# Optimization experiments

Measured on AMD Instinct MI355X. Metric: run time of the kernel, lower is better.

The kernel has to match this reference:

```python
import jax, jax.numpy as jnp
import numpy as np
import math

INPUT_FRAMES = 12
FUTURE_FRAMES = 26
T_STEPS = INPUT_FRAMES + FUTURE_FRAMES - 1  # 37
HD = 64   # hidden_dim
D = 16    # d_attn
CIN = 3   # input channels (time='stable')
COUT = 2  # output_dim
H, W = 24, 48


def conv2d(x, w, b, pad):
    # x: (N,C,H,W), w: (O,I,kh,kw)
    y = jax.lax.conv_general_dilated(x, w, (1, 1), [(pad, pad), (pad, pad)],
                                     dimension_numbers=('NCHW', 'OIHW', 'NCHW'))
    return y + b[None, :, None, None]


def spatial_attn(q, k, v):
    # q,k,v: (N,C,S); attention over spatial dim S
    scale = 1.0 / math.sqrt(q.shape[1])
    scores = jnp.einsum('ncs,nct->nst', q, k) * scale  # (N,S,S)
    a = jax.nn.softmax(scores, axis=-1)
    return jnp.einsum('nst,nct->ncs', a, v)


def setup_inputs() -> dict:
    key = jax.random.key(0)
    ks = jax.random.split(key, 8)
    s = 0.05
    inp = {
        'input_x': jax.random.normal(ks[0], (16, T_STEPS, H, W, CIN), dtype=jnp.float32),
        # ConvLSTM gate conv: in = CIN+HD, out = 4*HD, 3x3
        'conv_w': jax.random.normal(ks[1], (4 * HD, CIN + HD, 3, 3), dtype=jnp.float32) * s,
        'conv_b': jnp.zeros((4 * HD,), jnp.float32),
        # SA memory module
        'h_w': jax.random.normal(ks[2], (3 * D, HD, 1, 1), dtype=jnp.float32) * s,
        'h_b': jnp.zeros((3 * D,), jnp.float32),
        'm_w': jax.random.normal(ks[3], (2 * D, HD, 1, 1), dtype=jnp.float32) * s,
        'm_b': jnp.zeros((2 * D,), jnp.float32),
        'z_w': jax.random.normal(ks[4], (D, 2 * D, 1, 1), dtype=jnp.float32) * s,
        'z_b': jnp.zeros((D,), jnp.float32),
        'o_w': jax.random.normal(ks[5], (3 * HD, HD + D, 3, 3), dtype=jnp.float32) * s,
        'o_b': jnp.zeros((3 * HD,), jnp.float32),
        # final 1x1 projection to output_dim
        'out_w': jax.random.normal(ks[6], (COUT, HD, 1, 1), dtype=jnp.float32) * s,
        'out_b': jnp.zeros((COUT,), jnp.float32),
    }
    return inp


def reference(input_x, conv_w, conv_b, h_w, h_b, m_w, m_b, z_w, z_b, o_w, o_b, out_w, out_b):
    x = jnp.transpose(input_x, (0, 1, 4, 2, 3))  # (N,T,C,H,W)
    N = x.shape[0]
    S = H * W

    h0 = jnp.zeros((N, HD, H, W), x.dtype)
    carry0 = (h0, h0, h0, jnp.zeros((N, COUT, H, W), x.dtype))

    def step(carry, inp_t):
        h, c, m, prev_out = carry
        xt, t = inp_t  # xt: (N,CIN,H,W), t: scalar
        autoreg = jnp.concatenate([prev_out, xt[:, 2:]], axis=1)
        feed = jnp.where(t < INPUT_FRAMES, xt, autoreg)
        # ConvLSTM gates
        comb = conv2d(jnp.concatenate([feed, h], axis=1), conv_w, conv_b, 1)
        ci, cf, co, cg = jnp.split(comb, 4, axis=1)
        i = jax.nn.sigmoid(ci)
        f = jax.nn.sigmoid(cf)
        o = jax.nn.sigmoid(co)
        g = jnp.tanh(cg)
        c = f * c + i * g
        h = o * jnp.tanh(c)
        # self-attention memory
        hq, hk, hv = jnp.split(conv2d(h, h_w, h_b, 0), 3, axis=1)
        mk, mv = jnp.split(conv2d(m, m_w, m_b, 0), 2, axis=1)
        Zh = spatial_attn(hq.reshape(N, D, S), hk.reshape(N, D, S), hv.reshape(N, D, S))
        Zm = spatial_attn(hq.reshape(N, D, S), mk.reshape(N, D, S), mv.reshape(N, D, S))
        Z = conv2d(jnp.concatenate([Zh.reshape(N, D, H, W), Zm.reshape(N, D, H, W)], axis=1), z_w, z_b, 0)
        iog = conv2d(jnp.concatenate([Z, h], axis=1), o_w, o_b, 1)
        si, sg, so = jnp.split(iog, 3, axis=1)
        si = jax.nn.sigmoid(si)
        sg = jnp.tanh(sg)
        m = si * sg + (1.0 - si) * m
        h = jax.nn.sigmoid(so) * m
        out = conv2d(h, out_w, out_b, 0)
        return (h, c, m, out), out

    xs = (jnp.transpose(x, (1, 0, 2, 3, 4)), jnp.arange(T_STEPS))
    _, outs = jax.lax.scan(step, carry0, xs)
    outputs = jnp.transpose(outs, (1, 0, 2, 3, 4))  # (N,T,COUT,H,W)

    nino = outputs[:, -FUTURE_FRAMES:, 0, 10:13, 19:30].mean(axis=(2, 3))  # (N,26)
    nino_pred = (nino[:, :-2] + nino[:, 1:-1] + nino[:, 2:]) / 3.0          # (N,24)
    return outputs, nino_pred
```

## Files before the change

### kernel.cpp

```cpp
#include <hip/hip_runtime.h>
#include <math.h>

#define HD 64
#define DATT 16
#define NCIN 3
#define NCOUT 2
#define HH 24
#define WW 48
#define SS (HH*WW)
#define NB 16
#define TSTEPS 37
#define INPUT_FRAMES 12

#define PR 26
#define PC 52
#define PHW (PR*PC)

#define OFF_H     0
#define OFF_C     1384448
#define OFF_M     2564096
#define OFF_FEED  3743744
#define OFF_Z     3808640
#define ZERO_END  4154752
#define OFF_QKV   4154752
#define OFF_MKV   5039488
#define OFF_HB    5629312
#define OFF_IOG   8873344
#define OFF_BF2   12412288
#define OFF_BF    12596864

typedef __attribute__((ext_vector_type(8))) short short8;
typedef __attribute__((ext_vector_type(4))) float f32x4;

__device__ __forceinline__ float sigmoidf_(float x) {
    return 1.0f / (1.0f + __expf(-x));
}
__device__ __forceinline__ unsigned short f2bf(float f) {
    unsigned u = __float_as_uint(f);
    unsigned r = (u + 0x7fffu + ((u >> 16) & 1u)) >> 16;
    return (unsigned short)r;
}
__device__ __forceinline__ float bf2f(unsigned short b) {
    return __uint_as_float(((unsigned)b) << 16);
}
__device__ __forceinline__ unsigned packbf(float f) {
    unsigned short hi = f2bf(f);
    unsigned short lo = f2bf(f - bf2f(hi));
    return ((unsigned)lo << 16) | (unsigned)hi;
}
__device__ __forceinline__ float unpackbf(unsigned pk) {
    return __uint_as_float(pk << 16) + __uint_as_float(pk & 0xffff0000u);
}
__device__ __forceinline__ unsigned cvt_pk_bf16(float a, float b) {
    unsigned r;
    asm("v_cvt_pk_bf16_f32 %0, %1, %2" : "=v"(r) : "v"(a), "v"(b));
    return r;
}
__device__ __forceinline__ int permrow(int t) {
    int kb = t >> 5, tl = t & 31;
    int quad = tl >> 3, rr = tl & 7;
    return kb * 32 + ((rr >= 4) ? 16 : 0) + quad * 4 + (rr & 3);
}

#define MKFRAG(P0, P1, ah, al) do {                                  \
    ah.i[0] = (P0.y << 16) | (P0.x & 0xffff);                        \
    ah.i[1] = (P0.w << 16) | (P0.z & 0xffff);                        \
    ah.i[2] = (P1.y << 16) | (P1.x & 0xffff);                        \
    ah.i[3] = (P1.w << 16) | (P1.z & 0xffff);                        \
    al.i[0] = (P0.y & 0xffff0000) | ((unsigned)P0.x >> 16);          \
    al.i[1] = (P0.w & 0xffff0000) | ((unsigned)P0.z >> 16);          \
    al.i[2] = (P1.y & 0xffff0000) | ((unsigned)P1.x >> 16);          \
    al.i[3] = (P1.w & 0xffff0000) | ((unsigned)P1.z >> 16);          \
} while (0)

__global__ void k_zero(float* __restrict__ p, int n4) {
    int i = blockIdx.x * blockDim.x + threadIdx.x;
    if (i < n4) ((float4*)p)[i] = make_float4(0.f, 0.f, 0.f, 0.f);
}

__global__ void k_prep_bf2(const float* __restrict__ cw, unsigned short* __restrict__ bbuf) {
    int idx = blockIdx.x * 256 + threadIdx.x;
    if (idx >= 344064) return;
    int j    = idx & 7;
    int lane = (idx >> 3) & 63;
    int ki   = (idx >> 9) % 21;
    int nt   = (idx / 10752) % 16;
    int p    = idx / 172032;
    int k = ki * 32 + (lane >> 4) * 8 + j;
    int ncol = nt * 16 + (lane & 15);
    unsigned short v = 0;
    if (k < 648) {
        int c = k % 72, kt = k / 72;
        if (c < 67) {
            float w = cw[ncol * 603 + c * 9 + kt];
            unsigned short hi = f2bf(w);
            v = (p == 0) ? hi : f2bf(w - bf2f(hi));
        }
    }
    bbuf[idx] = v;
}

__global__ void k_prep_bf(const float* __restrict__ ow, unsigned short* __restrict__ bbuf) {
    int idx = blockIdx.x * 256 + threadIdx.x;
    if (idx >= 282624) return;
    int j    = idx & 7;
    int lane = (idx >> 3) & 63;
    int ki   = (idx >> 9) % 23;
    int nt   = (idx / 11776) % 12;
    int p    = idx / 141312;
    int k = ki * 32 + (lane >> 4) * 8 + j;
    int ncol = nt * 16 + (lane & 15);
    unsigned short v = 0;
    if (k < 720) {
        int c = k % 80, kt = k / 80;
        float w = ow[ncol * 720 + c * 9 + kt];
        unsigned short hi = f2bf(w);
        v = (p == 0) ? hi : f2bf(w - bf2f(hi));
    }
    bbuf[idx] = v;
}

__global__ void k_feed0(const float* __restrict__ x, unsigned* __restrict__ feed) {
    int i = blockIdx.x * blockDim.x + threadIdx.x;
    if (i >= NB * 3 * SS) return;
    int s = i % SS;
    int ch = (i / SS) % 3;
    int n = i / (3 * SS);
    int y = s / WW, xx = s % WW;
    float v = x[(((size_t)(n * TSTEPS + 0) * HH + y) * WW + xx) * NCIN + ch];
    feed[((size_t)(n * 3 + ch) * PR + (y + 1)) * PC + (xx + 1)] = packbf(v);
}

#define ASTR2 76
#define ZOFF2 (3*52*ASTR2)
__global__ __launch_bounds__(256) void k_conv_lstm_mfma(
    const unsigned* __restrict__ feed, const unsigned* __restrict__ hin,
    const unsigned short* __restrict__ bbuf, const float* __restrict__ cb,
    float* __restrict__ c, unsigned* __restrict__ hout)
{
    __shared__ __align__(16) int lds[3 * 52 * ASTR2 + 8];
    const int y0 = blockIdx.x;
    const int nb = blockIdx.y;
    const int n  = blockIdx.z;
    const int tid = threadIdx.x;

    const unsigned* fbase = feed + (size_t)n * 3 * PHW;
    const unsigned* hbase = hin + (size_t)n * HD * PHW;
    for (int e = tid; e < 2808; e += 256) {
        int grp = e / 156;
        int r2  = e - grp * 156;
        int pr = r2 / 52, pc = r2 - pr * 52;
        int cc0 = grp * 4;
        int vv[4];
#pragma unroll
        for (int j = 0; j < 4; ++j) {
            int cc = cc0 + j;
            int t = 0;
            if (cc < 3)        t = (int)fbase[(size_t)cc * PHW + (y0 + pr) * PC + pc];
            else if (cc < 67)  t = (int)hbase[(size_t)(cc - 3) * PHW + (y0 + pr) * PC + pc];
            vv[j] = t;
        }
        int4 v; v.x = vv[0]; v.y = vv[1]; v.z = vv[2]; v.w = vv[3];
        *(int4*)&lds[r2 * ASTR2 + cc0] = v;
    }
    if (tid < 8) lds[ZOFF2 + tid] = 0;
    __syncthreads();

    const int wv = tid >> 6;
    const int lane = tid & 63;
    const int mcol = lane & 15;
    const int quad = lane >> 4;

    f32x4 acc[2][3];
#pragma unroll
    for (int jg = 0; jg < 2; ++jg)
#pragma unroll
        for (int xt = 0; xt < 3; ++xt) acc[jg][xt] = (f32x4){0.f, 0.f, 0.f, 0.f};

    const unsigned short* b0 = bbuf + ((size_t)(wv * 4 + nb * 2 + 0) * 21) * 512 + lane * 8;
    const unsigned short* b1 = bbuf + ((size_t)(wv * 4 + nb * 2 + 1) * 21) * 512 + lane * 8;

    short8 cb0h = *(const short8*)(b0);
    short8 cb0l = *(const short8*)(b0 + 172032);
    short8 cb1h = *(const short8*)(b1);
    short8 cb1l = *(const short8*)(b1 + 172032);

    for (int ki = 0; ki < 21; ++ki) {
        int kn = (ki < 20) ? (ki + 1) * 512 : 20 * 512;
        short8 nb0h = *(const short8*)(b0 + kn);
        short8 nb0l = *(const short8*)(b0 + kn + 172032);
        short8 nb1h = *(const short8*)(b1 + kn);
        short8 nb1l = *(const short8*)(b1 + kn + 172032);

        int k0 = ki * 32 + quad * 8;
        int ab, step;
        if (k0 < 648) {
            int kt = k0 / 72;
            int c0 = k0 - kt * 72;
            int dy = kt / 3, dx = kt - dy * 3;
            ab = (dy * 52 + mcol + dx) * ASTR2 + c0;
            step = 16 * ASTR2;
        } else {
            ab = ZOFF2; step = 0;
        }
        int4 A0 = *(const int4*)&lds[ab],            A1 = *(const int4*)&lds[ab + 4];
        int4 B0 = *(const int4*)&lds[ab + step],     B1 = *(const int4*)&lds[ab + step + 4];
        int4 C0 = *(const int4*)&lds[ab + 2 * step], C1 = *(const int4*)&lds[ab + 2 * step + 4];

        union { int i[4]; short8 v; } ah, al;
        MKFRAG(A0, A1, ah, al);
        acc[0][0] = __builtin_amdgcn_mfma_f32_16x16x32_bf16(ah.v, cb0h, acc[0][0], 0, 0, 0);
        acc[0][0] = __builtin_amdgcn_mfma_f32_16x16x32_bf16(ah.v, cb0l, acc[0][0], 0, 0, 0);
        acc[0][0] = __builtin_amdgcn_mfma_f32_16x16x32_bf16(al.v, cb0h, acc[0][0], 0, 0, 0);
        acc[1][0] = __builtin_amdgcn_mfma_f32_16x16x32_bf16(ah.v, cb1h, acc[1][0], 0, 0, 0);
        acc[1][0] = __builtin_amdgcn_mfma_f32_16x16x32_bf16(ah.v, cb1l, acc[1][0], 0, 0, 0);
        acc[1][0] = __builtin_amdgcn_mfma_f32_16x16x32_bf16(al.v, cb1h, acc[1][0], 0, 0, 0);
        MKFRAG(B0, B1, ah, al);
        acc[0][1] = __builtin_amdgcn_mfma_f32_16x16x32_bf16(ah.v, cb0h, acc[0][1], 0, 0, 0);
        acc[0][1] = __builtin_amdgcn_mfma_f32_16x16x32_bf16(ah.v, cb0l, acc[0][1], 0, 0, 0);
        acc[0][1] = __builtin_amdgcn_mfma_f32_16x16x32_bf16(al.v, cb0h, acc[0][1], 0, 0, 0);
        acc[1][1] = __builtin_amdgcn_mfma_f32_16x16x32_bf16(ah.v, cb1h, acc[1][1], 0, 0, 0);
        acc[1][1] = __builtin_amdgcn_mfma_f32_16x16x32_bf16(ah.v, cb1l, acc[1][1], 0, 0, 0);
        acc[1][1] = __builtin_amdgcn_mfma_f32_16x16x32_bf16(al.v, cb1h, acc[1][1], 0, 0, 0);
        MKFRAG(C0, C1, ah, al);
        acc[0][2] = __builtin_amdgcn_mfma_f32_16x16x32_bf16(ah.v, cb0h, acc[0][2], 0, 0, 0);
        acc[0][2] = __builtin_amdgcn_mfma_f32_16x16x32_bf16(ah.v, cb0l, acc[0][2], 0, 0, 0);
        acc[0][2] = __builtin_amdgcn_mfma_f32_16x16x32_bf16(al.v, cb0h, acc[0][2], 0, 0, 0);
        acc[1][2] = __builtin_amdgcn_mfma_f32_16x16x32_bf16(ah.v, cb1h, acc[1][2], 0, 0, 0);
        acc[1][2] = __builtin_amdgcn_mfma_f32_16x16x32_bf16(ah.v, cb1l, acc[1][2], 0, 0, 0);
        acc[1][2] = __builtin_amdgcn_mfma_f32_16x16x32_bf16(al.v, cb1h, acc[1][2], 0, 0, 0);

        cb0h = nb0h; cb0l = nb0l; cb1h = nb1h; cb1l = nb1l;
    }

    __syncthreads();
    float* exch = (float*)lds;
#pragma unroll
    for (int jg = 0; jg < 2; ++jg)
#pragma unroll
        for (int xt = 0; xt < 3; ++xt)
#pragma unroll
            for (int r = 0; r < 4; ++r)
                exch[((wv * 2 + jg) * 3 + xt) * 272 + (quad * 4 + r) * 17 + mcol] = acc[jg][xt][r];
    __syncthreads();

    const int ch32 = tid & 31;
    const int xg = tid >> 5;
    const int jg = ch32 >> 4, col = ch32 & 15;
    const int gch = nb * 32 + ch32;
    const float bi = cb[gch], bfv = cb[64 + gch], bo = cb[128 + gch], bg = cb[192 + gch];
    size_t cbase = ((size_t)(n * HD + gch) * HH + y0) * WW;
    unsigned* hp = hout + ((size_t)(n * HD + gch) * PR + y0 + 1) * PC + 1;
#pragma unroll
    for (int k = 0; k < 6; ++k) {
        int x = xg * 6 + k;
        int xt = x >> 4, row = x & 15;
        float iv = sigmoidf_(exch[((0 * 2 + jg) * 3 + xt) * 272 + row * 17 + col] + bi);
        float fv = sigmoidf_(exch[((1 * 2 + jg) * 3 + xt) * 272 + row * 17 + col] + bfv);
        float ov = sigmoidf_(exch[((2 * 2 + jg) * 3 + xt) * 272 + row * 17 + col] + bo);
        float gv = tanhf    (exch[((3 * 2 + jg) * 3 + xt) * 272 + row * 17 + col] + bg);
        float cold = c[cbase + x];
        float cn = fv * cold + iv * gv;
        float hn = ov * tanhf(cn);
        c[cbase + x] = cn;
        hp[x] = packbf(hn);
    }
}

#define ASTR (84)
#define ZOFF (3*52*ASTR)
__global__ __launch_bounds__(192) void k_conv_sa(
    const unsigned* __restrict__ Zin, const unsigned* __restrict__ hin,
    const unsigned short* __restrict__ bbuf, const float* __restrict__ ob,
    float* __restrict__ m, unsigned* __restrict__ hout)
{
    __shared__ __align__(16) int lds[3 * 52 * ASTR + 8];
    const int y0 = blockIdx.x;
    const int cbk = blockIdx.y;
    const int n  = blockIdx.z;
    const int tid = threadIdx.x;

    const unsigned* zbase = Zin + (size_t)n * DATT * PHW;
    const unsigned* hbase = hin + (size_t)n * HD * PHW;
    for (int e = tid; e < 3120; e += 192) {
        int grp = e / 156;
        int r2  = e - grp * 156;
        int pr = r2 / 52, pc = r2 - pr * 52;
        int cc0 = grp * 4;
        int vv[4];
#pragma unroll
        for (int j = 0; j < 4; ++j) {
            int cc = cc0 + j;
            const unsigned* src = (cc < 16) ? (zbase + (size_t)cc * PHW)
                                            : (hbase + (size_t)(cc - 16) * PHW);
            vv[j] = (int)src[(y0 + pr) * PC + pc];
        }
        int4 v; v.x = vv[0]; v.y = vv[1]; v.z = vv[2]; v.w = vv[3];
        *(int4*)&lds[r2 * ASTR + cc0] = v;
    }
    if (tid < 8) lds[ZOFF + tid] = 0;
    __syncthreads();

    const int wv = tid >> 6;
    const int lane = tid & 63;
    const int mcol = lane & 15;
    const int quad = lane >> 4;

    f32x4 acc[2][3];
#pragma unroll
    for (int j = 0; j < 2; ++j)
#pragma unroll
        for (int xt = 0; xt < 3; ++xt) acc[j][xt] = (f32x4){0.f, 0.f, 0.f, 0.f};

    const unsigned short* b0 = bbuf + ((size_t)(wv * 4 + cbk * 2 + 0) * 23) * 512 + lane * 8;
    const unsigned short* b1 = bbuf + ((size_t)(wv * 4 + cbk * 2 + 1) * 23) * 512 + lane * 8;

    short8 cb0h = *(const short8*)(b0);
    short8 cb0l = *(const short8*)(b0 + 141312);
    short8 cb1h = *(const short8*)(b1);
    short8 cb1l = *(const short8*)(b1 + 141312);

    for (int ki = 0; ki < 23; ++ki) {
        int kn = (ki < 22) ? (ki + 1) * 512 : 22 * 512;
        short8 nb0h = *(const short8*)(b0 + kn);
        short8 nb0l = *(const short8*)(b0 + kn + 141312);
        short8 nb1h = *(const short8*)(b1 + kn);
        short8 nb1l = *(const short8*)(b1 + kn + 141312);

        int k0 = ki * 32 + quad * 8;
        int ab, step;
        if (k0 < 720) {
            int kt = k0 / 80;
            int c0 = k0 - kt * 80;
            int dy = kt / 3, dx = kt - dy * 3;
            ab = (dy * 52 + mcol + dx) * ASTR + c0;
            step = 16 * ASTR;
        } else {
            ab = ZOFF; step = 0;
        }
        int4 A0 = *(const int4*)&lds[ab],            A1 = *(const int4*)&lds[ab + 4];
        int4 B0 = *(const int4*)&lds[ab + step],     B1 = *(const int4*)&lds[ab + step + 4];
        int4 C0 = *(const int4*)&lds[ab + 2 * step], C1 = *(const int4*)&lds[ab + 2 * step + 4];

        union { int i[4]; short8 v; } ah, al;
        MKFRAG(A0, A1, ah, al);
        acc[0][0] = __builtin_amdgcn_mfma_f32_16x16x32_bf16(ah.v, cb0h, acc[0][0], 0, 0, 0);
        acc[0][0] = __builtin_amdgcn_mfma_f32_16x16x32_bf16(ah.v, cb0l, acc[0][0], 0, 0, 0);
        acc[0][0] = __builtin_amdgcn_mfma_f32_16x16x32_bf16(al.v, cb0h, acc[0][0], 0, 0, 0);
        acc[1][0] = __builtin_amdgcn_mfma_f32_16x16x32_bf16(ah.v, cb1h, acc[1][0], 0, 0, 0);
        acc[1][0] = __builtin_amdgcn_mfma_f32_16x16x32_bf16(ah.v, cb1l, acc[1][0], 0, 0, 0);
        acc[1][0] = __builtin_amdgcn_mfma_f32_16x16x32_bf16(al.v, cb1h, acc[1][0], 0, 0, 0);
        MKFRAG(B0, B1, ah, al);
        acc[0][1] = __builtin_amdgcn_mfma_f32_16x16x32_bf16(ah.v, cb0h, acc[0][1], 0, 0, 0);
        acc[0][1] = __builtin_amdgcn_mfma_f32_16x16x32_bf16(ah.v, cb0l, acc[0][1], 0, 0, 0);
        acc[0][1] = __builtin_amdgcn_mfma_f32_16x16x32_bf16(al.v, cb0h, acc[0][1], 0, 0, 0);
        acc[1][1] = __builtin_amdgcn_mfma_f32_16x16x32_bf16(ah.v, cb1h, acc[1][1], 0, 0, 0);
        acc[1][1] = __builtin_amdgcn_mfma_f32_16x16x32_bf16(ah.v, cb1l, acc[1][1], 0, 0, 0);
        acc[1][1] = __builtin_amdgcn_mfma_f32_16x16x32_bf16(al.v, cb1h, acc[1][1], 0, 0, 0);
        MKFRAG(C0, C1, ah, al);
        acc[0][2] = __builtin_amdgcn_mfma_f32_16x16x32_bf16(ah.v, cb0h, acc[0][2], 0, 0, 0);
        acc[0][2] = __builtin_amdgcn_mfma_f32_16x16x32_bf16(ah.v, cb0l, acc[0][2], 0, 0, 0);
        acc[0][2] = __builtin_amdgcn_mfma_f32_16x16x32_bf16(al.v, cb0h, acc[0][2], 0, 0, 0);
        acc[1][2] = __builtin_amdgcn_mfma_f32_16x16x32_bf16(ah.v, cb1h, acc[1][2], 0, 0, 0);
        acc[1][2] = __builtin_amdgcn_mfma_f32_16x16x32_bf16(ah.v, cb1l, acc[1][2], 0, 0, 0);
        acc[1][2] = __builtin_amdgcn_mfma_f32_16x16x32_bf16(al.v, cb1h, acc[1][2], 0, 0, 0);

        cb0h = nb0h; cb0l = nb0l; cb1h = nb1h; cb1l = nb1l;
    }

    __syncthreads();
    float* exch = (float*)lds;
#pragma unroll
    for (int j = 0; j < 2; ++j)
#pragma unroll
        for (int xt = 0; xt < 3; ++xt)
#pragma unroll
            for (int r = 0; r < 4; ++r)
                exch[((wv * 2 + j) * 3 + xt) * 272 + (quad * 4 + r) * 17 + mcol] = acc[j][xt][r];
    __syncthreads();

    const int ch32 = tid & 31;
    const int xg = tid >> 5;
    const int jg = ch32 >> 4, col = ch32 & 15;
    const int gch = cbk * 32 + ch32;
    const float bsi = ob[gch], bsg = ob[64 + gch], bso = ob[128 + gch];
    float* mrow = m + ((size_t)(n * HD + gch) * HH + y0) * WW;
    unsigned* hp = hout + ((size_t)(n * HD + gch) * PR + y0 + 1) * PC + 1;
#pragma unroll
    for (int k = 0; k < 8; ++k) {
        int x = xg * 8 + k;
        int xt = x >> 4, row = x & 15;
        float si = sigmoidf_(exch[((0 * 2 + jg) * 3 + xt) * 272 + row * 17 + col] + bsi);
        float sg = tanhf    (exch[((1 * 2 + jg) * 3 + xt) * 272 + row * 17 + col] + bsg);
        float so =           exch[((2 * 2 + jg) * 3 + xt) * 272 + row * 17 + col] + bso;
        float mo = mrow[x];
        float mn = si * sg + (1.f - si) * mo;
        mrow[x] = mn;
        hp[x] = packbf(sigmoidf_(so) * mn);
    }
}

__global__ __launch_bounds__(256) void k_qkv(
    const unsigned* __restrict__ h, const float* __restrict__ m,
    const float* __restrict__ hw, const float* __restrict__ hb,
    const float* __restrict__ mw, const float* __restrict__ mb,
    unsigned short* __restrict__ pl) {
    __shared__ float lw[512];
    __shared__ float lb[8];
    const int g = blockIdx.y;
    const int tid = threadIdx.x;
    const float* wsrc = (g < 6) ? (hw + g * 512) : (mw + (g - 6) * 512);
    const float* bsrc = (g < 6) ? (hb + g * 8) : (mb + (g - 6) * 8);
    for (int i = tid; i < 512; i += 256) lw[i] = wsrc[i];
    if (tid < 8) lb[tid] = bsrc[tid];
    __syncthreads();

    int idx = blockIdx.x * 256 + tid;
    int s = idx % SS;
    int n = idx / SS;

    float reg[HD];
    if (g < 6) {
        int y = s / WW, x = s % WW;
        const unsigned* src = h + (size_t)n * HD * PHW + (y + 1) * PC + (x + 1);
#pragma unroll
        for (int ic = 0; ic < HD; ++ic) reg[ic] = unpackbf(src[ic * PHW]);
    } else {
        const float* src = m + (size_t)n * HD * SS + s;
#pragma unroll
        for (int ic = 0; ic < HD; ++ic) reg[ic] = src[ic * SS];
    }

    float out[8];
#pragma unroll
    for (int j = 0; j < 8; ++j) {
        const float* wr = &lw[j * HD];
        float a = lb[j];
#pragma unroll
        for (int ic = 0; ic < HD; ++ic) a += reg[ic] * wr[ic];
        out[j] = a;
    }

    unsigned short* bq  = pl;
    unsigned short* akh = pl + 294912;
    unsigned short* akm = pl + 589824;
    unsigned short* bvh = pl + 884736;
    unsigned short* bvm = pl + 1179648;
    const int c0 = (g & 1) * 8;

    if (g < 2) {
        unsigned w0 = (unsigned)f2bf(out[0]) | ((unsigned)f2bf(out[1]) << 16);
        unsigned w1 = (unsigned)f2bf(out[2]) | ((unsigned)f2bf(out[3]) << 16);
        unsigned w2 = (unsigned)f2bf(out[4]) | ((unsigned)f2bf(out[5]) << 16);
        unsigned w3 = (unsigned)f2bf(out[6]) | ((unsigned)f2bf(out[7]) << 16);
        *(uint4*)&bq[((size_t)n * SS + s) * 16 + c0] = make_uint4(w0, w1, w2, w3);
    } else if (g < 4 || (g >= 6 && g < 8)) {
        int row = permrow(s);
        unsigned short* base = (g < 4) ? akh : akm;
        unsigned w0 = (unsigned)f2bf(out[0]) | ((unsigned)f2bf(out[1]) << 16);
        unsigned w1 = (unsigned)f2bf(out[2]) | ((unsigned)f2bf(out[3]) << 16);
        unsigned w2 = (unsigned)f2bf(out[4]) | ((unsigned)f2bf(out[5]) << 16);
        unsigned w3 = (unsigned)f2bf(out[6]) | ((unsigned)f2bf(out[7]) << 16);
        *(uint4*)&base[((size_t)n * SS + row) * 16 + c0] = make_uint4(w0, w1, w2, w3);
    } else {
        unsigned short* base = (g < 6) ? bvh : bvm;
#pragma unroll
        for (int j = 0; j < 8; ++j)
            base[((size_t)n * 16 + c0 + j) * SS + s] = f2bf(out[j]);
    }
}

__global__ __launch_bounds__(256) void k_attn(
    const unsigned short* __restrict__ pl, const unsigned short* __restrict__ zbuf,
    const float* __restrict__ zw, const float* __restrict__ zb,
    unsigned* __restrict__ Z)
{
    __shared__ float ldsO[4][2][16][16];
    __shared__ float ldsF[2][16][16];
    __shared__ float ldsL[4][2][16];
    __shared__ float ldsLF[2][16];

    const int n   = blockIdx.x;
    const int qt  = blockIdx.y;
    const int tid = threadIdx.x;
    const int wv  = tid >> 6;
    const int lane = tid & 63;
    const int col  = lane & 15;
    const int quad = lane >> 4;
    const bool hi  = quad >= 2;

    const unsigned short* bq  = pl;
    const unsigned short* akh = pl + 294912;
    const unsigned short* akm = pl + 589824;
    const unsigned short* bvh = pl + 884736;
    const unsigned short* bvm = pl + 1179648;

    const size_t nb = (size_t)n * 18432;
    const int stepk = hi ? 0 : 512;
    const int subk  = hi ? 0 : 256;
    const unsigned short* qp  = hi ? zbuf : (bq  + nb + ((size_t)(qt * 16 + col)) * 16 + quad * 8);
    const unsigned short* khb = hi ? zbuf : (akh + nb + col * 16 + quad * 8);
    const unsigned short* kmb = hi ? zbuf : (akm + nb + col * 16 + quad * 8);
    const unsigned short* vhb = bvh + nb + (size_t)col * SS + quad * 8;
    const unsigned short* vmb = bvm + nb + (size_t)col * SS + quad * 8;

    short8 qf = *(const short8*)qp;

    f32x4 oh = (f32x4){0.f,0.f,0.f,0.f}, om = (f32x4){0.f,0.f,0.f,0.f};
    float lh = 0.f, lm = 0.f;
    const int kb0 = wv * 9, kb1 = kb0 + 9;
    for (int kb = kb0; kb < kb1; ++kb) {
        const unsigned short* kh0 = khb + (size_t)kb * stepk;
        const unsigned short* km0 = kmb + (size_t)kb * stepk;
        short8 khA = *(const short8*)kh0;
        short8 khB = *(const short8*)(kh0 + subk);
        short8 kmA = *(const short8*)km0;
        short8 kmB = *(const short8*)(km0 + subk);
        short8 vh  = *(const short8*)(vhb + (size_t)kb * 32);
        short8 vm  = *(const short8*)(vmb + (size_t)kb * 32);
        const f32x4 z4 = (f32x4){0.f,0.f,0.f,0.f};
        f32x4 sA = __builtin_amdgcn_mfma_f32_16x16x32_bf16(khA, qf, z4, 0, 0, 0);
        f32x4 sB = __builtin_amdgcn_mfma_f32_16x16x32_bf16(khB, qf, z4, 0, 0, 0);
        f32x4 tA = __builtin_amdgcn_mfma_f32_16x16x32_bf16(kmA, qf, z4, 0, 0, 0);
        f32x4 tB = __builtin_amdgcn_mfma_f32_16x16x32_bf16(kmB, qf, z4, 0, 0, 0);

        float pa0 = __expf(0.25f * sA[0]), pa1 = __expf(0.25f * sA[1]);
        float pa2 = __expf(0.25f * sA[2]), pa3 = __expf(0.25f * sA[3]);
        float pb0 = __expf(0.25f * sB[0]), pb1 = __expf(0.25f * sB[1]);
        float pb2 = __expf(0.25f * sB[2]), pb3 = __expf(0.25f * sB[3]);
        lh += (pa0 + pa1 + pa2 + pa3) + (pb0 + pb1 + pb2 + pb3);
        union { unsigned u[4]; short8 v; } ph;
        ph.u[0] = cvt_pk_bf16(pa0, pa1); ph.u[1] = cvt_pk_bf16(pa2, pa3);
        ph.u[2] = cvt_pk_bf16(pb0, pb1); ph.u[3] = cvt_pk_bf16(pb2, pb3);
        oh = __builtin_amdgcn_mfma_f32_16x16x32_bf16(ph.v, vh, oh, 0, 0, 0);

        float qa0 = __expf(0.25f * tA[0]), qa1 = __expf(0.25f * tA[1]);
        float qa2 = __expf(0.25f * tA[2]), qa3 = __expf(0.25f * tA[3]);
        float qb0 = __expf(0.25f * tB[0]), qb1 = __expf(0.25f * tB[1]);
        float qb2 = __expf(0.25f * tB[2]), qb3 = __expf(0.25f * tB[3]);
        lm += (qa0 + qa1 + qa2 + qa3) + (qb0 + qb1 + qb2 + qb3);
        union { unsigned u[4]; short8 v; } pm;
        pm.u[0] = cvt_pk_bf16(qa0, qa1); pm.u[1] = cvt_pk_bf16(qa2, qa3);
        pm.u[2] = cvt_pk_bf16(qb0, qb1); pm.u[3] = cvt_pk_bf16(qb2, qb3);
        om = __builtin_amdgcn_mfma_f32_16x16x32_bf16(pm.v, vm, om, 0, 0, 0);
    }

    lh += __shfl_xor(lh, 16); lh += __shfl_xor(lh, 32);
    lm += __shfl_xor(lm, 16); lm += __shfl_xor(lm, 32);

#pragma unroll
    for (int r = 0; r < 4; ++r) {
        ldsO[wv][0][quad * 4 + r][col] = oh[r];
        ldsO[wv][1][quad * 4 + r][col] = om[r];
    }
    if (lane < 16) { ldsL[wv][0][lane] = lh; ldsL[wv][1][lane] = lm; }
    __syncthreads();

    if (tid < 128) {
        int a_ = tid >> 6, rem = tid & 63, q_ = rem >> 2, j4 = (rem & 3) * 4;
        float4 s4 = make_float4(0.f, 0.f, 0.f, 0.f);
#pragma unroll
        for (int w = 0; w < 4; ++w) {
            float4 v = *(const float4*)&ldsO[w][a_][q_][j4];
            s4.x += v.x; s4.y += v.y; s4.z += v.z; s4.w += v.w;
        }
        *(float4*)&ldsF[a_][q_][j4] = s4;
    } else if (tid < 160) {
        int e = tid - 128, a_ = e >> 4, q_ = e & 15;
        ldsLF[a_][q_] = ldsL[0][a_][q_] + ldsL[1][a_][q_] +
                        ldsL[2][a_][q_] + ldsL[3][a_][q_];
    }
    __syncthreads();

    const int q  = tid & 15;
    const int zc = tid >> 4;
    float iLh = 1.f / ldsLF[0][q], iLm = 1.f / ldsLF[1][q];
    const float* zr = zw + zc * 32;
    float a = zb[zc];
#pragma unroll
    for (int j = 0; j < 16; ++j)
        a += zr[j] * (ldsF[0][q][j] * iLh) + zr[16 + j] * (ldsF[1][q][j] * iLm);
    int s = qt * 16 + q;
    int y = s / WW, x = s % WW;
    Z[((size_t)(n * DATT + zc) * PR + y + 1) * PC + x + 1] = packbf(a);
}

__global__ void k_out_feed(const unsigned* __restrict__ h, const float* __restrict__ ow,
                           const float* __restrict__ ob, const float* __restrict__ x,
                           float* __restrict__ outbuf, unsigned* __restrict__ feed, int t) {
    int idx = blockIdx.x * 256 + threadIdx.x;
    if (idx >= NB * SS) return;
    int s = idx % SS;
    int n = idx / SS;
    int y = s / WW, xx = s % WW;
    const unsigned* src = h + (size_t)n * HD * PHW + (y + 1) * PC + (xx + 1);
    float o0 = ob[0], o1 = ob[1];
#pragma unroll
    for (int ic = 0; ic < HD; ++ic) {
        float r = unpackbf(src[ic * PHW]);
        o0 += r * ow[ic];
        o1 += r * ow[HD + ic];
    }
    outbuf[(((size_t)n * TSTEPS + t) * NCOUT + 0) * SS + s] = o0;
    outbuf[(((size_t)n * TSTEPS + t) * NCOUT + 1) * SS + s] = o1;

    if (t + 1 < TSTEPS) {
        int t1 = t + 1;
        const float* xp = &x[(((size_t)(n * TSTEPS + t1) * HH + y) * WW + xx) * NCIN];
        float f0, f1, f2 = xp[2];
        if (t1 < INPUT_FRAMES) { f0 = xp[0]; f1 = xp[1]; }
        else { f0 = o0; f1 = o1; }
        size_t fb = ((size_t)(n * 3 + 0) * PR + y + 1) * PC + xx + 1;
        feed[fb] = packbf(f0);
        feed[fb + PHW] = packbf(f1);
        feed[fb + 2 * (size_t)PHW] = packbf(f2);
    }
}

__global__ void k_nino(const float* __restrict__ outbuf, float* __restrict__ pred) {
    int tidx = threadIdx.x;
    if (tidx >= 16 * 24) return;
    int j = tidx % 24;
    int n = tidx / 24;
    float acc = 0.f;
    for (int f = j; f < j + 3; ++f) {
        int t = 11 + f;
        const float* p = &outbuf[(((size_t)n * TSTEPS + t) * NCOUT + 0) * SS];
        float sloc = 0.f;
        for (int y = 10; y <= 12; ++y)
            for (int x = 19; x <= 29; ++x)
                sloc += p[y * WW + x];
        acc += sloc * (1.f / 33.f);
    }
    pred[n * 24 + j] = acc * (1.f / 3.f);
}

extern "C" void kernel_launch(void* const* d_in, const int* in_sizes, int n_in,
                              void* d_out, int out_size, void* d_ws, size_t ws_size,
                              hipStream_t stream) {
    const float* x      = (const float*)d_in[0];
    const float* conv_w = (const float*)d_in[1];
    const float* conv_b = (const float*)d_in[2];
    const float* h_w    = (const float*)d_in[3];
    const float* h_b    = (const float*)d_in[4];
    const float* m_w    = (const float*)d_in[5];
    const float* m_b    = (const float*)d_in[6];
    const float* z_w    = (const float*)d_in[7];
    const float* z_b    = (const float*)d_in[8];
    const float* o_w    = (const float*)d_in[9];
    const float* o_b    = (const float*)d_in[10];
    const float* out_w  = (const float*)d_in[11];
    const float* out_b  = (const float*)d_in[12];

    float* ws   = (float*)d_ws;
    unsigned* hA    = (unsigned*)(ws + OFF_H);
    float* c    = ws + OFF_C;
    float* m    = ws + OFF_M;
    unsigned* feedp = (unsigned*)(ws + OFF_FEED);
    unsigned* Zp    = (unsigned*)(ws + OFF_Z);
    unsigned* hB    = (unsigned*)(ws + OFF_HB);
    unsigned short* bf2 = (unsigned short*)(ws + OFF_BF2);
    unsigned short* bf  = (unsigned short*)(ws + OFF_BF);
    unsigned short* planes = (unsigned short*)(ws + OFF_QKV);
    const unsigned short* zbuf = (const unsigned short*)(ws + OFF_MKV);
    float* outp = (float*)d_out;

    k_zero<<<4058, 256, 0, stream>>>(ws, 1038688);
    k_zero<<<1352, 256, 0, stream>>>(ws + OFF_HB, 346112);
    k_zero<<<1, 64, 0, stream>>>(ws + OFF_MKV, 16);
    k_prep_bf2<<<1344, 256, 0, stream>>>(conv_w, bf2);
    k_prep_bf<<<1104, 256, 0, stream>>>(o_w, bf);
    k_feed0<<<216, 256, 0, stream>>>(x, feedp);

    for (int t = 0; t < TSTEPS; ++t) {
        k_conv_lstm_mfma<<<dim3(24, 2, 16), 256, 0, stream>>>(feedp, hB, bf2, conv_b, c, hA);
        k_qkv<<<dim3(72, 10), 256, 0, stream>>>(hA, m, h_w, h_b, m_w, m_b, planes);
        k_attn<<<dim3(16, 72), 256, 0, stream>>>(planes, zbuf, z_w, z_b, Zp);
        k_conv_sa<<<dim3(24, 2, 16), 192, 0, stream>>>(Zp, hA, bf, o_b, m, hB);
        k_out_feed<<<72, 256, 0, stream>>>(hB, out_w, out_b, x, outp, feedp, t);
    }
    k_nino<<<1, 384, 0, stream>>>(outp, outp + (size_t)NB * TSTEPS * NCOUT * SS);
}
```

Before: 3.915 ms.

## Process two output rows per ConvLSTM block and deepen weight prefetch

Each k_conv_lstm_mfma block now computes two image rows instead of one, staging four padded input rows in LDS so every weight fragment loaded from global memory feeds twice as many MFMAs. The grid halves to 12x2x16, which cuts the weight traffic per step, and the gate epilogue handles 12 positions per thread. Both conv kernels also prefetch weight fragments two K-iterations ahead instead of one. In exchange, register pressure (12 accumulators) and LDS use go up, and fewer blocks are launched (384), which may lower occupancy and fill on the GPU.

Result: slower. 4.552 ms (+16.3%).

```diff
diff --git a/kernel.cpp b/kernel.cpp
--- a/kernel.cpp
+++ b/kernel.cpp
@@ -132,13 +132,13 @@
 }
 
 #define ASTR2 76
-#define ZOFF2 (3*52*ASTR2)
+#define ZOFF2 (4*52*ASTR2)
 __global__ __launch_bounds__(256) void k_conv_lstm_mfma(
     const unsigned* __restrict__ feed, const unsigned* __restrict__ hin,
     const unsigned short* __restrict__ bbuf, const float* __restrict__ cb,
     float* __restrict__ c, unsigned* __restrict__ hout)
 {
-    __shared__ __align__(16) int lds[3 * 52 * ASTR2 + 8];
+    __shared__ __align__(16) int lds[4 * 52 * ASTR2 + 80 + 8];
     const int y0 = blockIdx.x;
     const int nb = blockIdx.y;
     const int n  = blockIdx.z;
@@ -146,7 +146,145 @@
 
     const unsigned* fbase = feed + (size_t)n * 3 * PHW;
     const unsigned* hbase = hin + (size_t)n * HD * PHW;
-    for (int e = tid; e < 2808; e += 256) {
+    for (int e = tid; e < 3744; e += 256) {
+        int grp = e / 208;
+        int r2  = e - grp * 208;
+        int pr = r2 / 52, pc = r2 - pr * 52;
+        int cc0 = grp * 4;
+        int vv[4];
+#pragma unroll
+        for (int j = 0; j < 4; ++j) {
+            int cc = cc0 + j;
+            int t = 0;
+            if (cc < 3)        t = (int)fbase[(size_t)cc * PHW + (2 * y0 + pr) * PC + pc];
+            else if (cc < 67)  t = (int)hbase[(size_t)(cc - 3) * PHW + (2 * y0 + pr) * PC + pc];
+            vv[j] = t;
+        }
+        int4 v; v.x = vv[0]; v.y = vv[1]; v.z = vv[2]; v.w = vv[3];
+        *(int4*)&lds[r2 * ASTR2 + cc0] = v;
+    }
+    if (tid < 80) lds[ZOFF2 + tid] = 0;
+    __syncthreads();
+
+    const int wv = tid >> 6;
+    const int lane = tid & 63;
+    const int mcol = lane & 15;
+    const int quad = lane >> 4;
+
+    f32x4 acc[2][6];
+#pragma unroll
+    for (int jg = 0; jg < 2; ++jg)
+#pragma unroll
+        for (int st = 0; st < 6; ++st) acc[jg][st] = (f32x4){0.f, 0.f, 0.f, 0.f};
+
+    const unsigned short* b0 = bbuf + ((size_t)(wv * 4 + nb * 2 + 0) * 21) * 512 + lane * 8;
+    const unsigned short* b1 = bbuf + ((size_t)(wv * 4 + nb * 2 + 1) * 21) * 512 + lane * 8;
+
+    short8 cb0h = *(const short8*)(b0);
+    short8 cb0l = *(const short8*)(b0 + 172032);
+    short8 cb1h = *(const short8*)(b1);
+    short8 cb1l = *(const short8*)(b1 + 172032);
+    short8 pb0h = *(const short8*)(b0 + 512);
+    short8 pb0l = *(const short8*)(b0 + 512 + 172032);
+    short8 pb1h = *(const short8*)(b1 + 512);
+    short8 pb1l = *(const short8*)(b1 + 512 + 172032);
+
+    for (int ki = 0; ki < 21; ++ki) {
+        int kn = (ki + 2 <= 20) ? (ki + 2) * 512 : 20 * 512;
+        short8 qb0h = *(const short8*)(b0 + kn);
+        short8 qb0l = *(const short8*)(b0 + kn + 172032);
+        short8 qb1h = *(const short8*)(b1 + kn);
+        short8 qb1l = *(const short8*)(b1 + kn + 172032);
+
+        int k0 = ki * 32 + quad * 8;
+        int ab, stepx, stepy;
+        if (k0 < 648) {
+            int kt = k0 / 72;
+            int c0 = k0 - kt * 72;
+            int dy = kt / 3, dx = kt - dy * 3;
+            ab = (dy * 52 + mcol + dx) * ASTR2 + c0;
+            stepx = 16 * ASTR2;
+            stepy = 52 * ASTR2;
+        } else {
+            ab = ZOFF2; stepx = 0; stepy = 0;
+        }
+
+#pragma unroll
+        for (int yy = 0; yy < 2; ++yy) {
+#pragma unroll
+            for (int xt = 0; xt < 3; ++xt) {
+                int abase = ab + yy * stepy + xt * stepx;
+                int4 P0 = *(const int4*)&lds[abase];
+                int4 P1 = *(const int4*)&lds[abase + 4];
+                union { int i[4]; short8 v; } ah, al;
+                MKFRAG(P0, P1, ah, al);
+                const int st = yy * 3 + xt;
+                acc[0][st] = __builtin_amdgcn_mfma_f32_16x16x32_bf16(ah.v, cb0h, acc[0][st], 0, 0, 0);
+                acc[0][st] = __builtin_amdgcn_mfma_f32_16x16x32_bf16(ah.v, cb0l, acc[0][st], 0, 0, 0);
+                acc[0][st] = __builtin_amdgcn_mfma_f32_16x16x32_bf16(al.v, cb0h, acc[0][st], 0, 0, 0);
+                acc[1][st] = __builtin_amdgcn_mfma_f32_16x16x32_bf16(ah.v, cb1h, acc[1][st], 0, 0, 0);
+                acc[1][st] = __builtin_amdgcn_mfma_f32_16x16x32_bf16(ah.v, cb1l, acc[1][st], 0, 0, 0);
+                acc[1][st] = __builtin_amdgcn_mfma_f32_16x16x32_bf16(al.v, cb1h, acc[1][st], 0, 0, 0);
+            }
+        }
+
+        cb0h = pb0h; cb0l = pb0l; cb1h = pb1h; cb1l = pb1l;
+        pb0h = qb0h; pb0l = qb0l; pb1h = qb1h; pb1l = qb1l;
+    }
+
+    __syncthreads();
+    float* exch = (float*)lds;
+#pragma unroll
+    for (int jg = 0; jg < 2; ++jg)
+#pragma unroll
+        for (int st = 0; st < 6; ++st)
+#pragma unroll
+            for (int r = 0; r < 4; ++r)
+                exch[((wv * 2 + jg) * 6 + st) * 272 + (quad * 4 + r) * 17 + mcol] = acc[jg][st][r];
+    __syncthreads();
+
+    const int ch32 = tid & 31;
+    const int xg = tid >> 5;
+    const int jg = ch32 >> 4, col = ch32 & 15;
+    const int gch = nb * 32 + ch32;
+    const float bi = cb[gch], bfv = cb[64 + gch], bo = cb[128 + gch], bg = cb[192 + gch];
+#pragma unroll
+    for (int k = 0; k < 12; ++k) {
+        int pos = xg * 12 + k;
+        int yy = pos / 48;
+        int x = pos - yy * 48;
+        int xt = x >> 4, row = x & 15;
+        int st = yy * 3 + xt;
+        float iv = sigmoidf_(exch[((0 * 2 + jg) * 6 + st) * 272 + row * 17 + col] + bi);
+        float fv = sigmoidf_(exch[((1 * 2 + jg) * 6 + st) * 272 + row * 17 + col] + bfv);
+        float ov = sigmoidf_(exch[((2 * 2 + jg) * 6 + st) * 272 + row * 17 + col] + bo);
+        float gv = tanhf    (exch[((3 * 2 + jg) * 6 + st) * 272 + row * 17 + col] + bg);
+        int ya = 2 * y0 + yy;
+        size_t ci = ((size_t)(n * HD + gch) * HH + ya) * WW + x;
+        float cold = c[ci];
+        float cn = fv * cold + iv * gv;
+        float hn = ov * tanhf(cn);
+        c[ci] = cn;
+        hout[((size_t)(n * HD + gch) * PR + ya + 1) * PC + x + 1] = packbf(hn);
+    }
+}
+
+#define ASTR (84)
+#define ZOFF (3*52*ASTR)
+__global__ __launch_bounds__(192) void k_conv_sa(
+    const unsigned* __restrict__ Zin, const unsigned* __restrict__ hin,
+    const unsigned short* __restrict__ bbuf, const float* __restrict__ ob,
+    float* __restrict__ m, unsigned* __restrict__ hout)
+{
+    __shared__ __align__(16) int lds[3 * 52 * ASTR + 8];
+    const int y0 = blockIdx.x;
+    const int cbk = blockIdx.y;
+    const int n  = blockIdx.z;
+    const int tid = threadIdx.x;
+
+    const unsigned* zbase = Zin + (size_t)n * DATT * PHW;
+    const unsigned* hbase = hin + (size_t)n * HD * PHW;
+    for (int e = tid; e < 3120; e += 192) {
         int grp = e / 156;
         int r2  = e - grp * 156;
         int pr = r2 / 52, pc = r2 - pr * 52;
@@ -155,15 +293,14 @@
 #pragma unroll
         for (int j = 0; j < 4; ++j) {
             int cc = cc0 + j;
-            int t = 0;
-            if (cc < 3)        t = (int)fbase[(size_t)cc * PHW + (y0 + pr) * PC + pc];
-            else if (cc < 67)  t = (int)hbase[(size_t)(cc - 3) * PHW + (y0 + pr) * PC + pc];
-            vv[j] = t;
+            const unsigned* src = (cc < 16) ? (zbase + (size_t)cc * PHW)
+                                            : (hbase + (size_t)(cc - 16) * PHW);
+            vv[j] = (int)src[(y0 + pr) * PC + pc];
         }
         int4 v; v.x = vv[0]; v.y = vv[1]; v.z = vv[2]; v.w = vv[3];
-        *(int4*)&lds[r2 * ASTR2 + cc0] = v;
-    }
-    if (tid < 8) lds[ZOFF2 + tid] = 0;
+        *(int4*)&lds[r2 * ASTR + cc0] = v;
+    }
+    if (tid < 8) lds[ZOFF + tid] = 0;
     __syncthreads();
 
     const int wv = tid >> 6;
@@ -173,35 +310,39 @@
 
     f32x4 acc[2][3];
 #pragma unroll
-    for (int jg = 0; jg < 2; ++jg)
-#pragma unroll
-        for (int xt = 0; xt < 3; ++xt) acc[jg][xt] = (f32x4){0.f, 0.f, 0.f, 0.f};
-
-    const unsigned short* b0 = bbuf + ((size_t)(wv * 4 + nb * 2 + 0) * 21) * 512 + lane * 8;
-    const unsigned short* b1 = bbuf + ((size_t)(wv * 4 + nb * 2 + 1) * 21) * 512 + lane * 8;
+    for (int j = 0; j < 2; ++j)
+#pragma unroll
+        for (int xt = 0; xt < 3; ++xt) acc[j][xt] = (f32x4){0.f, 0.f, 0.f, 0.f};
+
+    const unsigned short* b0 = bbuf + ((size_t)(wv * 4 + cbk * 2 + 0) * 23) * 512 + lane * 8;
+    const unsigned short* b1 = bbuf + ((size_t)(wv * 4 + cbk * 2 + 1) * 23) * 512 + lane * 8;
 
     short8 cb0h = *(const short8*)(b0);
-    short8 cb0l = *(const short8*)(b0 + 172032);
+    short8 cb0l = *(const short8*)(b0 + 141312);
     short8 cb1h = *(const short8*)(b1);
-    short8 cb1l = *(const short8*)(b1 + 172032);
-
-    for (int ki = 0; ki < 21; ++ki) {
-        int kn = (ki < 20) ? (ki + 1) * 512 : 20 * 512;
-        short8 nb0h = *(const short8*)(b0 + kn);
-        short8 nb0l = *(const short8*)(b0 + kn + 172032);
-        short8 nb1h = *(const short8*)(b1 + kn);
-        short8 nb1l = *(const short8*)(b1 + kn + 172032);
+    short8 cb1l = *(const short8*)(b1 + 141312);
+    short8 pb0h = *(const short8*)(b0 + 512);
+    short8 pb0l = *(const short8*)(b0 + 512 + 141312);
+    short8 pb1h = *(const short8*)(b1 + 512);
+    short8 pb1l = *(const short8*)(b1 + 512 + 141312);
+
+    for (int ki = 0; ki < 23; ++ki) {
+        int kn = (ki + 2 <= 22) ? (ki + 2) * 512 : 22 * 512;
+        short8 qb0h = *(const short8*)(b0 + kn);
+        short8 qb0l = *(const short8*)(b0 + kn + 141312);
+        short8 qb1h = *(const short8*)(b1 + kn);
+        short8 qb1l = *(const short8*)(b1 + kn + 141312);
 
         int k0 = ki * 32 + quad * 8;
         int ab, step;
-        if (k0 < 648) {
-            int kt = k0 / 72;
-            int c0 = k0 - kt * 72;
+        if (k0 < 720) {
+            int kt = k0 / 80;
+            int c0 = k0 - kt * 80;
             int dy = kt / 3, dx = kt - dy * 3;
-            ab = (dy * 52 + mcol + dx) * ASTR2 + c0;
-            step = 16 * ASTR2;
+            ab = (dy * 52 + mcol + dx) * ASTR + c0;
+            step = 16 * ASTR;
         } else {
-            ab = ZOFF2; step = 0;
+            ab = ZOFF; step = 0;
         }
         int4 A0 = *(const int4*)&lds[ab],            A1 = *(const int4*)&lds[ab + 4];
         int4 B0 = *(const int4*)&lds[ab + step],     B1 = *(const int4*)&lds[ab + step + 4];
@@ -230,142 +371,8 @@
         acc[1][2] = __builtin_amdgcn_mfma_f32_16x16x32_bf16(ah.v, cb1l, acc[1][2], 0, 0, 0);
         acc[1][2] = __builtin_amdgcn_mfma_f32_16x16x32_bf16(al.v, cb1h, acc[1][2], 0, 0, 0);
 
-        cb0h = nb0h; cb0l = nb0l; cb1h = nb1h; cb1l = nb1l;
-    }
-
-    __syncthreads();
-    float* exch = (float*)lds;
-#pragma unroll
-    for (int jg = 0; jg < 2; ++jg)
-#pragma unroll
-        for (int xt = 0; xt < 3; ++xt)
-#pragma unroll
-            for (int r = 0; r < 4; ++r)
-                exch[((wv * 2 + jg) * 3 + xt) * 272 + (quad * 4 + r) * 17 + mcol] = acc[jg][xt][r];
-    __syncthreads();
-
-    const int ch32 = tid & 31;
-    const int xg = tid >> 5;
-    const int jg = ch32 >> 4, col = ch32 & 15;
-    const int gch = nb * 32 + ch32;
-    const float bi = cb[gch], bfv = cb[64 + gch], bo = cb[128 + gch], bg = cb[192 + gch];
-    size_t cbase = ((size_t)(n * HD + gch) * HH + y0) * WW;
-    unsigned* hp = hout + ((size_t)(n * HD + gch) * PR + y0 + 1) * PC + 1;
-#pragma unroll
-    for (int k = 0; k < 6; ++k) {
-        int x = xg * 6 + k;
-        int xt = x >> 4, row = x & 15;
-        float iv = sigmoidf_(exch[((0 * 2 + jg) * 3 + xt) * 272 + row * 17 + col] + bi);
-        float fv = sigmoidf_(exch[((1 * 2 + jg) * 3 + xt) * 272 + row * 17 + col] + bfv);
-        float ov = sigmoidf_(exch[((2 * 2 + jg) * 3 + xt) * 272 + row * 17 + col] + bo);
-        float gv = tanhf    (exch[((3 * 2 + jg) * 3 + xt) * 272 + row * 17 + col] + bg);
-        float cold = c[cbase + x];
-        float cn = fv * cold + iv * gv;
-        float hn = ov * tanhf(cn);
-        c[cbase + x] = cn;
-        hp[x] = packbf(hn);
-    }
-}
-
-#define ASTR (84)
-#define ZOFF (3*52*ASTR)
-__global__ __launch_bounds__(192) void k_conv_sa(
-    const unsigned* __restrict__ Zin, const unsigned* __restrict__ hin,
-    const unsigned short* __restrict__ bbuf, const float* __restrict__ ob,
-    float* __restrict__ m, unsigned* __restrict__ hout)
-{
-    __shared__ __align__(16) int lds[3 * 52 * ASTR + 8];
-    const int y0 = blockIdx.x;
-    const int cbk = blockIdx.y;
-    const int n  = blockIdx.z;
-    const int tid = threadIdx.x;
-
-    const unsigned* zbase = Zin + (size_t)n * DATT * PHW;
-    const unsigned* hbase = hin + (size_t)n * HD * PHW;
-    for (int e = tid; e < 3120; e += 192) {
-        int grp = e / 156;
-        int r2  = e - grp * 156;
-        int pr = r2 / 52, pc = r2 - pr * 52;
-        int cc0 = grp * 4;
-        int vv[4];
-#pragma unroll
-        for (int j = 0; j < 4; ++j) {
-            int cc = cc0 + j;
-            const unsigned* src = (cc < 16) ? (zbase + (size_t)cc * PHW)
-                                            : (hbase + (size_t)(cc - 16) * PHW);
-            vv[j] = (int)src[(y0 + pr) * PC + pc];
-        }
-        int4 v; v.x = vv[0]; v.y = vv[1]; v.z = vv[2]; v.w = vv[3];
-        *(int4*)&lds[r2 * ASTR + cc0] = v;
-    }
-    if (tid < 8) lds[ZOFF + tid] = 0;
-    __syncthreads();
-
-    const int wv = tid >> 6;
-    const int lane = tid & 63;
-    const int mcol = lane & 15;
-    const int quad = lane >> 4;
-
-    f32x4 acc[2][3];
-#pragma unroll
-    for (int j = 0; j < 2; ++j)
-#pragma unroll
-        for (int xt = 0; xt < 3; ++xt) acc[j][xt] = (f32x4){0.f, 0.f, 0.f, 0.f};
-
-    const unsigned short* b0 = bbuf + ((size_t)(wv * 4 + cbk * 2 + 0) * 23) * 512 + lane * 8;
-    const unsigned short* b1 = bbuf + ((size_t)(wv * 4 + cbk * 2 + 1) * 23) * 512 + lane * 8;
-
-    short8 cb0h = *(const short8*)(b0);
-    short8 cb0l = *(const short8*)(b0 + 141312);
-    short8 cb1h = *(const short8*)(b1);
-    short8 cb1l = *(const short8*)(b1 + 141312);
-
-    for (int ki = 0; ki < 23; ++ki) {
-        int kn = (ki < 22) ? (ki + 1) * 512 : 22 * 512;
-        short8 nb0h = *(const short8*)(b0 + kn);
-        short8 nb0l = *(const short8*)(b0 + kn + 141312);
-        short8 nb1h = *(const short8*)(b1 + kn);
-        short8 nb1l = *(const short8*)(b1 + kn + 141312);
-
-        int k0 = ki * 32 + quad * 8;
-        int ab, step;
-        if (k0 < 720) {
-            int kt = k0 / 80;
-            int c0 = k0 - kt * 80;
-            int dy = kt / 3, dx = kt - dy * 3;
-            ab = (dy * 52 + mcol + dx) * ASTR + c0;
-            step = 16 * ASTR;
-        } else {
-            ab = ZOFF; step = 0;
-        }
-        int4 A0 = *(const int4*)&lds[ab],            A1 = *(const int4*)&lds[ab + 4];
-        int4 B0 = *(const int4*)&lds[ab + step],     B1 = *(const int4*)&lds[ab + step + 4];
-        int4 C0 = *(const int4*)&lds[ab + 2 * step], C1 = *(const int4*)&lds[ab + 2 * step + 4];
-
-        union { int i[4]; short8 v; } ah, al;
-        MKFRAG(A0, A1, ah, al);
-        acc[0][0] = __builtin_amdgcn_mfma_f32_16x16x32_bf16(ah.v, cb0h, acc[0][0], 0, 0, 0);
-        acc[0][0] = __builtin_amdgcn_mfma_f32_16x16x32_bf16(ah.v, cb0l, acc[0][0], 0, 0, 0);
-        acc[0][0] = __builtin_amdgcn_mfma_f32_16x16x32_bf16(al.v, cb0h, acc[0][0], 0, 0, 0);
-        acc[1][0] = __builtin_amdgcn_mfma_f32_16x16x32_bf16(ah.v, cb1h, acc[1][0], 0, 0, 0);
-        acc[1][0] = __builtin_amdgcn_mfma_f32_16x16x32_bf16(ah.v, cb1l, acc[1][0], 0, 0, 0);
-        acc[1][0] = __builtin_amdgcn_mfma_f32_16x16x32_bf16(al.v, cb1h, acc[1][0], 0, 0, 0);
-        MKFRAG(B0, B1, ah, al);
-        acc[0][1] = __builtin_amdgcn_mfma_f32_16x16x32_bf16(ah.v, cb0h, acc[0][1], 0, 0, 0);
-        acc[0][1] = __builtin_amdgcn_mfma_f32_16x16x32_bf16(ah.v, cb0l, acc[0][1], 0, 0, 0);
-        acc[0][1] = __builtin_amdgcn_mfma_f32_16x16x32_bf16(al.v, cb0h, acc[0][1], 0, 0, 0);
-        acc[1][1] = __builtin_amdgcn_mfma_f32_16x16x32_bf16(ah.v, cb1h, acc[1][1], 0, 0, 0);
-        acc[1][1] = __builtin_amdgcn_mfma_f32_16x16x32_bf16(ah.v, cb1l, acc[1][1], 0, 0, 0);
-        acc[1][1] = __builtin_amdgcn_mfma_f32_16x16x32_bf16(al.v, cb1h, acc[1][1], 0, 0, 0);
-        MKFRAG(C0, C1, ah, al);
-        acc[0][2] = __builtin_amdgcn_mfma_f32_16x16x32_bf16(ah.v, cb0h, acc[0][2], 0, 0, 0);
-        acc[0][2] = __builtin_amdgcn_mfma_f32_16x16x32_bf16(ah.v, cb0l, acc[0][2], 0, 0, 0);
-        acc[0][2] = __builtin_amdgcn_mfma_f32_16x16x32_bf16(al.v, cb0h, acc[0][2], 0, 0, 0);
-        acc[1][2] = __builtin_amdgcn_mfma_f32_16x16x32_bf16(ah.v, cb1h, acc[1][2], 0, 0, 0);
-        acc[1][2] = __builtin_amdgcn_mfma_f32_16x16x32_bf16(ah.v, cb1l, acc[1][2], 0, 0, 0);
-        acc[1][2] = __builtin_amdgcn_mfma_f32_16x16x32_bf16(al.v, cb1h, acc[1][2], 0, 0, 0);
-
-        cb0h = nb0h; cb0l = nb0l; cb1h = nb1h; cb1l = nb1l;
+        cb0h = pb0h; cb0l = pb0l; cb1h = pb1h; cb1l = pb1l;
+        pb0h = qb0h; pb0l = qb0l; pb1h = qb1h; pb1l = qb1l;
     }
 
     __syncthreads();
@@ -673,7 +680,7 @@
     k_feed0<<<216, 256, 0, stream>>>(x, feedp);
 
     for (int t = 0; t < TSTEPS; ++t) {
-        k_conv_lstm_mfma<<<dim3(24, 2, 16), 256, 0, stream>>>(feedp, hB, bf2, conv_b, c, hA);
+        k_conv_lstm_mfma<<<dim3(12, 2, 16), 256, 0, stream>>>(feedp, hB, bf2, conv_b, c, hA);
         k_qkv<<<dim3(72, 10), 256, 0, stream>>>(hA, m, h_w, h_b, m_w, m_b, planes);
         k_attn<<<dim3(16, 72), 256, 0, stream>>>(planes, zbuf, z_w, z_b, Zp);
         k_conv_sa<<<dim3(24, 2, 16), 192, 0, stream>>>(Zp, hA, bf, o_b, m, hB);
```
